# Kernel optimization log

Hardware: AMD Instinct MI355X
Metric: run time of the kernel (lower is better)

The kernel has to match this reference:

```python
import jax, jax.numpy as jnp
import numpy as np

B, S, D = 4, 2048, 1024
NEG_BIG = -1.0e9


def setup_inputs() -> dict:
    key = jax.random.key(0)
    ks = jax.random.split(key, 9)
    scale = 1.0 / np.sqrt(D)
    inp = {
        "v": jax.random.normal(ks[0], (B, S, D), dtype=jnp.float32),
        "k": jax.random.normal(ks[1], (B, S, D), dtype=jnp.float32),
        "q": jax.random.normal(ks[2], (B, S, D), dtype=jnp.float32),
        # causal mask: 1 where attention is disallowed (j > i), broadcast over batch
        "mask": jnp.triu(jnp.ones((1, S, S), dtype=jnp.float32), k=1),
        "Wq": jax.random.normal(ks[3], (D, D), dtype=jnp.float32) * scale,
        "bq": jnp.zeros((D,), dtype=jnp.float32),
        "Wk": jax.random.normal(ks[4], (D, D), dtype=jnp.float32) * scale,
        "bk": jnp.zeros((D,), dtype=jnp.float32),
        "Wv": jax.random.normal(ks[5], (D, D), dtype=jnp.float32) * scale,
        "bv": jnp.zeros((D,), dtype=jnp.float32),
    }
    return inp


def reference(v, k, q, mask, Wq, bq, Wk, bk, Wv, bv):
    # Dense projections (Keras Dense: x @ W + b)
    qp = q @ Wq + bq  # [B, S, D]
    kp = k @ Wk + bk  # [B, S, D]
    vp = v @ Wv + bv  # [B, S, D]

    dk = jnp.asarray(D, dtype=qp.dtype)
    logits = jnp.einsum("bqd,bkd->bqk", qp, kp) / jnp.sqrt(dk)  # [B, S, S]
    logits = logits + mask * NEG_BIG
    attn = jax.nn.softmax(logits, axis=-1)  # [B, S, S]
    out = jnp.einsum("bqk,bkd->bqd", attn, vp)  # [B, S, D]
    return out, attn
```

## Files before the change

### kernel.cpp

```cpp
#include <hip/hip_runtime.h>
#include <hip/hip_bf16.h>
#include <cstdint>

#define BATCH 4
#define S_LEN 2048
#define D_DIM 1024

typedef __attribute__((ext_vector_type(4))) float f32x4_t;
typedef __attribute__((ext_vector_type(8))) __bf16 bf16x8_t;

__device__ __forceinline__ ushort f32_to_bf16(float f) {
    uint32_t u = __float_as_uint(f);
    uint32_t r = (u + 0x7FFFu + ((u >> 16) & 1u)) >> 16;
    return (ushort)r;
}

__global__ __launch_bounds__(256)
void cvt3_kernel(const float* __restrict__ a, const float* __restrict__ b,
                 const float* __restrict__ c, ushort* __restrict__ out, int n4) {
    int z = blockIdx.y;
    const float* src = (z == 0) ? a : ((z == 1) ? b : c);
    ushort* dst = out + (size_t)z * n4 * 4;
    int idx = blockIdx.x * blockDim.x + threadIdx.x;
    int stride = gridDim.x * blockDim.x;
    const float4* in4 = (const float4*)src;
    ushort4* out4 = (ushort4*)dst;
    for (int i = idx; i < n4; i += stride) {
        float4 v = in4[i];
        ushort4 o;
        o.x = f32_to_bf16(v.x);
        o.y = f32_to_bf16(v.y);
        o.z = f32_to_bf16(v.z);
        o.w = f32_to_bf16(v.w);
        out4[i] = o;
    }
}

__global__ __launch_bounds__(256)
void transpose_cvt_kernel(const float* __restrict__ in, ushort* __restrict__ out,
                          int rows, int cols) {
    __shared__ ushort tile[64][66];
    int r0 = blockIdx.y * 64, c0 = blockIdx.x * 64;
    int t = threadIdx.x;
    int cr = t & 63;
    int cc = t >> 6;
    #pragma unroll
    for (int i = 0; i < 16; ++i) {
        int r = cc * 16 + i;
        tile[r][cr] = f32_to_bf16(in[(size_t)(r0 + r) * cols + (c0 + cr)]);
    }
    __syncthreads();
    #pragma unroll
    for (int i = 0; i < 16; ++i) {
        int c = cc * 16 + i;
        out[(size_t)(c0 + c) * rows + (r0 + cr)] = tile[cr][c];
    }
}

__global__ __launch_bounds__(256)
void transpose_bf16_kernel(const ushort* __restrict__ in, ushort* __restrict__ out,
                           int rows, int cols, int lda, long strideA, long strideB) {
    __shared__ ushort tile[64][66];
    const ushort* src = in + (size_t)blockIdx.z * strideA;
    ushort* dst = out + (size_t)blockIdx.z * strideB;
    int r0 = blockIdx.y * 64, c0 = blockIdx.x * 64;
    int t = threadIdx.x;
    int cr = t & 63;
    int cc = t >> 6;
    #pragma unroll
    for (int i = 0; i < 16; ++i) {
        int r = cc * 16 + i;
        tile[r][cr] = src[(size_t)(r0 + r) * lda + (c0 + cr)];
    }
    __syncthreads();
    #pragma unroll
    for (int i = 0; i < 16; ++i) {
        int c = cc * 16 + i;
        dst[(size_t)(c0 + c) * rows + (r0 + cr)] = tile[cr][c];
    }
}

enum { MODE_PROJ = 0, MODE_LOGITS = 1, MODE_OUT = 2 };

#define GBM 128
#define GBN 128
#define GBK 32

template<int MODE>
__global__ __launch_bounds__(256)
void gemm_bt_kernel(const ushort* __restrict__ A, const ushort* __restrict__ Bt,
                    const float* __restrict__ bias, void* __restrict__ Cout,
                    int K, int lda, int ldb, int ldc,
                    long strideA, long strideB, long strideC, float scale) {
    int bc = blockIdx.x, br = blockIdx.y, bz = blockIdx.z;
    if (MODE == MODE_LOGITS && bc > br) return;

    __shared__ ushort As[2][GBM * GBK];
    __shared__ ushort Bs[2][GBN * GBK];

    const ushort* Ab = (MODE == MODE_PROJ) ? A + (size_t)(bc >> 3) * strideA
                                           : A + (size_t)bz * strideA;
    const ushort* Bb = Bt + (size_t)bz * strideB;

    int brow = br * GBM, bcol = bc * GBN;
    int t = threadIdx.x;
    int lane = t & 63;
    int wave = t >> 6;
    int wr = wave >> 1, wc = wave & 1;

    int ksteps = K / GBK;
    if (MODE == MODE_OUT) ksteps = min(ksteps, (brow + GBM) / GBK);

    f32x4_t acc[4][4];
    #pragma unroll
    for (int m = 0; m < 4; ++m)
        #pragma unroll
        for (int n = 0; n < 4; ++n)
            acc[m][n] = (f32x4_t){0.f, 0.f, 0.f, 0.f};

    int row0 = t >> 2;
    int col0 = (t & 3) * 8;

    auto stage = [&](int kt, int buf) {
        int k0 = kt * GBK;
        #pragma unroll
        for (int i = 0; i < 2; ++i) {
            int row = i * 64 + row0;
            const ushort* srcA = Ab + (size_t)(brow + row) * lda + (k0 + col0);
            __builtin_amdgcn_global_load_lds(
                (const __attribute__((address_space(1))) uint32_t*)srcA,
                (__attribute__((address_space(3))) uint32_t*)&As[buf][(i * 256 + t) * 8],
                16, 0, 0);
            const ushort* srcB = Bb + (size_t)(bcol + row) * ldb + (k0 + col0);
            __builtin_amdgcn_global_load_lds(
                (const __attribute__((address_space(1))) uint32_t*)srcB,
                (__attribute__((address_space(3))) uint32_t*)&Bs[buf][(i * 256 + t) * 8],
                16, 0, 0);
        }
    };

    stage(0, 0);
    __syncthreads();

    for (int kt = 0; kt < ksteps; ++kt) {
        int cur = kt & 1;
        if (kt + 1 < ksteps) stage(kt + 1, cur ^ 1);

        bf16x8_t a_frag[4], b_frag[4];
        int arow = wr * 64 + (lane & 15);
        int kcol = (lane >> 4) * 8;
        #pragma unroll
        for (int m = 0; m < 4; ++m)
            a_frag[m] = *(const bf16x8_t*)&As[cur][(arow + m * 16) * GBK + kcol];
        int brl = wc * 64 + (lane & 15);
        #pragma unroll
        for (int n = 0; n < 4; ++n)
            b_frag[n] = *(const bf16x8_t*)&Bs[cur][(brl + n * 16) * GBK + kcol];

        __builtin_amdgcn_s_setprio(1);
        #pragma unroll
        for (int m = 0; m < 4; ++m)
            #pragma unroll
            for (int n = 0; n < 4; ++n)
                acc[m][n] = __builtin_amdgcn_mfma_f32_16x16x32_bf16(
                    a_frag[m], b_frag[n], acc[m][n], 0, 0, 0);
        __builtin_amdgcn_s_setprio(0);

        __syncthreads();
    }

    int crow0 = brow + wr * 64 + ((lane >> 4) * 4);
    int ccol0 = bcol + wc * 64 + (lane & 15);
    if (MODE == MODE_PROJ) {
        ushort* C = (ushort*)Cout;
        #pragma unroll
        for (int m = 0; m < 4; ++m) {
            #pragma unroll
            for (int n = 0; n < 4; ++n) {
                int col = ccol0 + n * 16;
                float bv = bias[col];
                #pragma unroll
                for (int j = 0; j < 4; ++j) {
                    int rowg = crow0 + m * 16 + j;
                    C[(size_t)rowg * ldc + col] = f32_to_bf16(acc[m][n][j] + bv);
                }
            }
        }
    } else {
        float* C = (float*)Cout + (size_t)bz * strideC;
        #pragma unroll
        for (int m = 0; m < 4; ++m)
            #pragma unroll
            for (int n = 0; n < 4; ++n) {
                int col = ccol0 + n * 16;
                #pragma unroll
                for (int j = 0; j < 4; ++j) {
                    int rowg = crow0 + m * 16 + j;
                    C[(size_t)rowg * ldc + col] = acc[m][n][j] * scale;
                }
            }
    }
}

__global__ __launch_bounds__(256)
void bias_concat_kernel(const float* __restrict__ bq, const float* __restrict__ bk,
                        const float* __restrict__ bv, float* __restrict__ out) {
    int i = blockIdx.x * blockDim.x + threadIdx.x;
    if (i < D_DIM) out[i] = bq[i];
    else if (i < 2 * D_DIM) out[i] = bk[i - D_DIM];
    else if (i < 3 * D_DIM) out[i] = bv[i - 2 * D_DIM];
}

__global__ __launch_bounds__(256)
void softmax_causal_kernel(float* __restrict__ attn, ushort* __restrict__ attn_bf) {
    int rowid = blockIdx.x;
    int i = rowid & (S_LEN - 1);
    float* lrow = attn + (size_t)rowid * S_LEN;
    ushort* brw = attn_bf + (size_t)rowid * S_LEN;
    int t = threadIdx.x;
    int nvalid = i + 1;

    float vals[8];
    float lmax = -1e30f;
    #pragma unroll
    for (int it = 0; it < 8; ++it) {
        int j = it * 256 + t;
        float v = (j < nvalid) ? lrow[j] : -1e30f;
        vals[it] = v;
        lmax = fmaxf(lmax, v);
    }
    #pragma unroll
    for (int off = 32; off > 0; off >>= 1)
        lmax = fmaxf(lmax, __shfl_xor(lmax, off));

    __shared__ float redm[4];
    __shared__ float reds[4];
    int wave = t >> 6, lane = t & 63;
    if (lane == 0) redm[wave] = lmax;
    __syncthreads();
    float m = fmaxf(fmaxf(redm[0], redm[1]), fmaxf(redm[2], redm[3]));

    float lsum = 0.f;
    #pragma unroll
    for (int it = 0; it < 8; ++it) {
        int j = it * 256 + t;
        float e = (j < nvalid) ? __expf(vals[it] - m) : 0.f;
        vals[it] = e;
        lsum += e;
    }
    #pragma unroll
    for (int off = 32; off > 0; off >>= 1)
        lsum += __shfl_xor(lsum, off);
    if (lane == 0) reds[wave] = lsum;
    __syncthreads();
    float denom = reds[0] + reds[1] + reds[2] + reds[3];
    float inv = 1.f / denom;

    #pragma unroll
    for (int it = 0; it < 8; ++it) {
        int j = it * 256 + t;
        float p = vals[it] * inv;
        lrow[j] = p;
        brw[j] = f32_to_bf16(p);
    }
}

extern "C" void kernel_launch(void* const* d_in, const int* in_sizes, int n_in,
                              void* d_out, int out_size, void* d_ws, size_t ws_size,
                              hipStream_t stream) {
    const float* v  = (const float*)d_in[0];
    const float* k  = (const float*)d_in[1];
    const float* q  = (const float*)d_in[2];
    const float* Wq = (const float*)d_in[4];
    const float* bq = (const float*)d_in[5];
    const float* Wk = (const float*)d_in[6];
    const float* bk = (const float*)d_in[7];
    const float* Wv = (const float*)d_in[8];
    const float* bv = (const float*)d_in[9];

    float* out  = (float*)d_out;
    float* attn = (float*)d_out + (size_t)BATCH * S_LEN * D_DIM;

    char* ws = (char*)d_ws;
    const size_t NTOK = (size_t)BATCH * S_LEN;
    const size_t XSZ  = NTOK * D_DIM * sizeof(ushort);
    ushort* xqkv  = (ushort*)(ws);
    ushort* qkvp  = (ushort*)(ws + 3 * XSZ);
    ushort* WT    = (ushort*)(ws + 6 * XSZ);
    float*  bias3 = (float*)(ws + 6 * XSZ + 3 * (size_t)D_DIM * D_DIM * sizeof(ushort));
    ushort* vpT     = (ushort*)(ws);
    ushort* attn_bf = (ushort*)(ws + XSZ);

    const int n4 = (int)(NTOK * D_DIM / 4);
    cvt3_kernel<<<dim3(1024, 3), dim3(256), 0, stream>>>(q, k, v, xqkv, n4);

    transpose_cvt_kernel<<<dim3(16, 16), dim3(256), 0, stream>>>(Wq, WT, D_DIM, D_DIM);
    transpose_cvt_kernel<<<dim3(16, 16), dim3(256), 0, stream>>>(Wk, WT + (size_t)D_DIM * D_DIM, D_DIM, D_DIM);
    transpose_cvt_kernel<<<dim3(16, 16), dim3(256), 0, stream>>>(Wv, WT + 2 * (size_t)D_DIM * D_DIM, D_DIM, D_DIM);
    bias_concat_kernel<<<dim3(12), dim3(256), 0, stream>>>(bq, bk, bv, bias3);

    dim3 pgrid(3 * D_DIM / GBN, (int)(NTOK / GBM), 1);
    gemm_bt_kernel<MODE_PROJ><<<pgrid, dim3(256), 0, stream>>>(
        xqkv, WT, bias3, qkvp, D_DIM, D_DIM, D_DIM, 3 * D_DIM,
        (long)NTOK * D_DIM, 0, 0, 1.f);

    transpose_bf16_kernel<<<dim3(D_DIM / 64, S_LEN / 64, BATCH), dim3(256), 0, stream>>>(
        qkvp + 2 * D_DIM, vpT, S_LEN, D_DIM, 3 * D_DIM,
        (long)S_LEN * 3 * D_DIM, (long)D_DIM * S_LEN);

    dim3 lgrid(S_LEN / GBN, S_LEN / GBM, BATCH);
    gemm_bt_kernel<MODE_LOGITS><<<lgrid, dim3(256), 0, stream>>>(
        qkvp, qkvp + D_DIM, nullptr, attn, D_DIM, 3 * D_DIM, 3 * D_DIM, S_LEN,
        (long)S_LEN * 3 * D_DIM, (long)S_LEN * 3 * D_DIM, (long)S_LEN * S_LEN, 0.03125f);

    softmax_causal_kernel<<<dim3((int)NTOK), dim3(256), 0, stream>>>(attn, attn_bf);

    dim3 ogrid(D_DIM / GBN, S_LEN / GBM, BATCH);
    gemm_bt_kernel<MODE_OUT><<<ogrid, dim3(256), 0, stream>>>(
        attn_bf, vpT, nullptr, out, S_LEN, S_LEN, S_LEN, D_DIM,
        (long)S_LEN * S_LEN, (long)D_DIM * S_LEN, (long)S_LEN * D_DIM, 1.f);
}
```

Baseline: 243.1 us.

## Rewrite GEMM with 256x128x64 tiles, 3-stage LDS pipeline and XOR swizzle

Replaces the 128x128x32 double-buffered GEMM with a 512-thread 256x128x64 tile kernel. It uses a triple-buffered LDS ring filled by async global_load_lds, XOR-swizzled LDS addressing to avoid bank conflicts, and split stage/compute phases with explicit waitcnt and barriers. The aim is more reuse per tile, better hiding of load latency, and less LDS bank-conflict stall. In exchange it uses much more LDS (occupancy 1), produces fewer blocks for the smaller GEMMs, and adds coarser causal skipping that wastes more work on the triangular logits.

```diff
diff --git a/kernel.cpp b/kernel.cpp
--- a/kernel.cpp
+++ b/kernel.cpp
@@ -80,103 +80,164 @@
     }
 }
 
+__global__ __launch_bounds__(256)
+void bias_concat_kernel(const float* __restrict__ bq, const float* __restrict__ bk,
+                        const float* __restrict__ bv, float* __restrict__ out) {
+    int i = blockIdx.x * blockDim.x + threadIdx.x;
+    if (i < D_DIM) out[i] = bq[i];
+    else if (i < 2 * D_DIM) out[i] = bk[i - D_DIM];
+    else if (i < 3 * D_DIM) out[i] = bv[i - 2 * D_DIM];
+}
+
 enum { MODE_PROJ = 0, MODE_LOGITS = 1, MODE_OUT = 2 };
 
-#define GBM 128
-#define GBN 128
-#define GBK 32
+#define BM 256
+#define BN 128
+#define BK 64
+#define NSLOT 3
 
 template<int MODE>
-__global__ __launch_bounds__(256)
-void gemm_bt_kernel(const ushort* __restrict__ A, const ushort* __restrict__ Bt,
-                    const float* __restrict__ bias, void* __restrict__ Cout,
-                    int K, int lda, int ldb, int ldc,
-                    long strideA, long strideB, long strideC, float scale) {
+__global__ __launch_bounds__(512, 1)
+void gemm3_kernel(const ushort* __restrict__ A, const ushort* __restrict__ Bt,
+                  const float* __restrict__ bias, void* __restrict__ Cout,
+                  int K, int lda, int ldb, int ldc,
+                  long strideA, long strideB, long strideC, float scale) {
     int bc = blockIdx.x, br = blockIdx.y, bz = blockIdx.z;
-    if (MODE == MODE_LOGITS && bc > br) return;
-
-    __shared__ ushort As[2][GBM * GBK];
-    __shared__ ushort Bs[2][GBN * GBK];
+    if (MODE == MODE_LOGITS && bc >= 2 * (br + 1)) return;
+
+    __shared__ ushort As[NSLOT][BM * BK];
+    __shared__ ushort Bs[NSLOT][BN * BK];
 
     const ushort* Ab = (MODE == MODE_PROJ) ? A + (size_t)(bc >> 3) * strideA
                                            : A + (size_t)bz * strideA;
     const ushort* Bb = Bt + (size_t)bz * strideB;
 
-    int brow = br * GBM, bcol = bc * GBN;
+    int brow = br * BM, bcol = bc * BN;
     int t = threadIdx.x;
     int lane = t & 63;
-    int wave = t >> 6;
-    int wr = wave >> 1, wc = wave & 1;
-
-    int ksteps = K / GBK;
-    if (MODE == MODE_OUT) ksteps = min(ksteps, (brow + GBM) / GBK);
-
-    f32x4_t acc[4][4];
-    #pragma unroll
-    for (int m = 0; m < 4; ++m)
-        #pragma unroll
-        for (int n = 0; n < 4; ++n)
+    int wid = t >> 6;
+    int wr = wid >> 2, wc = wid & 3;
+
+    int nkt = K / BK;
+    if (MODE == MODE_OUT) nkt = min(nkt, (brow + BM) / BK);
+
+    auto stageA = [&](int kt, int slot, int j) {
+        int o = (j * 512 + t) * 16;
+        int row = o >> 7;
+        int col = (o & 127) ^ ((row & 7) << 4);
+        const ushort* src = Ab + (size_t)(brow + row) * lda + kt * BK + (col >> 1);
+        __builtin_amdgcn_global_load_lds(
+            (const __attribute__((address_space(1))) uint32_t*)src,
+            (__attribute__((address_space(3))) uint32_t*)&As[slot][o >> 1],
+            16, 0, 0);
+    };
+    auto stageB = [&](int kt, int slot, int j) {
+        int o = (j * 512 + t) * 16;
+        int row = o >> 7;
+        int col = (o & 127) ^ ((row & 7) << 4);
+        const ushort* src = Bb + (size_t)(bcol + row) * ldb + kt * BK + (col >> 1);
+        __builtin_amdgcn_global_load_lds(
+            (const __attribute__((address_space(1))) uint32_t*)src,
+            (__attribute__((address_space(3))) uint32_t*)&Bs[slot][o >> 1],
+            16, 0, 0);
+    };
+
+    f32x4_t acc[8][2];
+    #pragma unroll
+    for (int m = 0; m < 8; ++m)
+        #pragma unroll
+        for (int n = 0; n < 2; ++n)
             acc[m][n] = (f32x4_t){0.f, 0.f, 0.f, 0.f};
 
-    int row0 = t >> 2;
-    int col0 = (t & 3) * 8;
-
-    auto stage = [&](int kt, int buf) {
-        int k0 = kt * GBK;
-        #pragma unroll
-        for (int i = 0; i < 2; ++i) {
-            int row = i * 64 + row0;
-            const ushort* srcA = Ab + (size_t)(brow + row) * lda + (k0 + col0);
-            __builtin_amdgcn_global_load_lds(
-                (const __attribute__((address_space(1))) uint32_t*)srcA,
-                (__attribute__((address_space(3))) uint32_t*)&As[buf][(i * 256 + t) * 8],
-                16, 0, 0);
-            const ushort* srcB = Bb + (size_t)(bcol + row) * ldb + (k0 + col0);
-            __builtin_amdgcn_global_load_lds(
-                (const __attribute__((address_space(1))) uint32_t*)srcB,
-                (__attribute__((address_space(3))) uint32_t*)&Bs[buf][(i * 256 + t) * 8],
-                16, 0, 0);
+    bf16x8_t af[4][2], bf[2][2];
+
+    auto readA = [&](int slot, int mh) {
+        #pragma unroll
+        for (int m = 0; m < 4; ++m) {
+            int ra = wr * 128 + mh * 64 + m * 16 + (lane & 15);
+            int sw = (ra & 7) << 4;
+            #pragma unroll
+            for (int ks = 0; ks < 2; ++ks) {
+                int cb = ks * 64 + ((lane >> 4) * 16);
+                af[m][ks] = *(const bf16x8_t*)((const char*)&As[slot][0] + ra * 128 + (cb ^ sw));
+            }
         }
     };
-
-    stage(0, 0);
-    __syncthreads();
-
-    for (int kt = 0; kt < ksteps; ++kt) {
-        int cur = kt & 1;
-        if (kt + 1 < ksteps) stage(kt + 1, cur ^ 1);
-
-        bf16x8_t a_frag[4], b_frag[4];
-        int arow = wr * 64 + (lane & 15);
-        int kcol = (lane >> 4) * 8;
+    auto readB = [&](int slot) {
+        #pragma unroll
+        for (int n = 0; n < 2; ++n) {
+            int rb = wc * 32 + n * 16 + (lane & 15);
+            int sw = (rb & 7) << 4;
+            #pragma unroll
+            for (int ks = 0; ks < 2; ++ks) {
+                int cb = ks * 64 + ((lane >> 4) * 16);
+                bf[n][ks] = *(const bf16x8_t*)((const char*)&Bs[slot][0] + rb * 128 + (cb ^ sw));
+            }
+        }
+    };
+
+    #pragma unroll
+    for (int j = 0; j < 4; ++j) stageA(0, 0, j);
+    stageB(0, 0, 0); stageB(0, 0, 1);
+    #pragma unroll
+    for (int j = 0; j < 4; ++j) stageA(1, 1, j);
+    stageB(1, 1, 0); stageB(1, 1, 1);
+    asm volatile("s_waitcnt vmcnt(6)" ::: "memory");
+    __builtin_amdgcn_sched_barrier(0);
+    __builtin_amdgcn_s_barrier();
+
+    int slot = 0;
+    for (int kt = 0; kt < nkt; ++kt) {
+        int sslot = slot + 2; if (sslot >= NSLOT) sslot -= NSLOT;
+        bool dostage = (kt + 2 < nkt);
+
+        if (dostage) { stageA(kt + 2, sslot, 0); stageA(kt + 2, sslot, 1); stageB(kt + 2, sslot, 0); }
+        readB(slot);
+        readA(slot, 0);
+        asm volatile("s_waitcnt lgkmcnt(0)" ::: "memory");
+        __builtin_amdgcn_sched_barrier(0);
+        __builtin_amdgcn_s_setprio(1);
         #pragma unroll
         for (int m = 0; m < 4; ++m)
-            a_frag[m] = *(const bf16x8_t*)&As[cur][(arow + m * 16) * GBK + kcol];
-        int brl = wc * 64 + (lane & 15);
-        #pragma unroll
-        for (int n = 0; n < 4; ++n)
-            b_frag[n] = *(const bf16x8_t*)&Bs[cur][(brl + n * 16) * GBK + kcol];
-
+            #pragma unroll
+            for (int n = 0; n < 2; ++n)
+                #pragma unroll
+                for (int ks = 0; ks < 2; ++ks)
+                    acc[m][n] = __builtin_amdgcn_mfma_f32_16x16x32_bf16(
+                        af[m][ks], bf[n][ks], acc[m][n], 0, 0, 0);
+        __builtin_amdgcn_s_setprio(0);
+        __builtin_amdgcn_s_barrier();
+
+        if (dostage) { stageA(kt + 2, sslot, 2); stageA(kt + 2, sslot, 3); stageB(kt + 2, sslot, 1); }
+        readA(slot, 1);
+        asm volatile("s_waitcnt lgkmcnt(0)" ::: "memory");
+        __builtin_amdgcn_sched_barrier(0);
         __builtin_amdgcn_s_setprio(1);
         #pragma unroll
         for (int m = 0; m < 4; ++m)
             #pragma unroll
-            for (int n = 0; n < 4; ++n)
-                acc[m][n] = __builtin_amdgcn_mfma_f32_16x16x32_bf16(
-                    a_frag[m], b_frag[n], acc[m][n], 0, 0, 0);
+            for (int n = 0; n < 2; ++n)
+                #pragma unroll
+                for (int ks = 0; ks < 2; ++ks)
+                    acc[4 + m][n] = __builtin_amdgcn_mfma_f32_16x16x32_bf16(
+                        af[m][ks], bf[n][ks], acc[4 + m][n], 0, 0, 0);
         __builtin_amdgcn_s_setprio(0);
-
-        __syncthreads();
-    }
-
-    int crow0 = brow + wr * 64 + ((lane >> 4) * 4);
-    int ccol0 = bcol + wc * 64 + (lane & 15);
+        if (dostage) { asm volatile("s_waitcnt vmcnt(6)" ::: "memory"); }
+        else         { asm volatile("s_waitcnt vmcnt(0)" ::: "memory"); }
+        __builtin_amdgcn_sched_barrier(0);
+        __builtin_amdgcn_s_barrier();
+
+        slot += 1; if (slot >= NSLOT) slot -= NSLOT;
+    }
+
+    int crow0 = brow + wr * 128 + ((lane >> 4) * 4);
+    int ccol0 = bcol + wc * 32 + (lane & 15);
     if (MODE == MODE_PROJ) {
         ushort* C = (ushort*)Cout;
         #pragma unroll
-        for (int m = 0; m < 4; ++m) {
-            #pragma unroll
-            for (int n = 0; n < 4; ++n) {
+        for (int m = 0; m < 8; ++m) {
+            #pragma unroll
+            for (int n = 0; n < 2; ++n) {
                 int col = ccol0 + n * 16;
                 float bv = bias[col];
                 #pragma unroll
@@ -189,9 +250,9 @@
     } else {
         float* C = (float*)Cout + (size_t)bz * strideC;
         #pragma unroll
-        for (int m = 0; m < 4; ++m)
-            #pragma unroll
-            for (int n = 0; n < 4; ++n) {
+        for (int m = 0; m < 8; ++m)
+            #pragma unroll
+            for (int n = 0; n < 2; ++n) {
                 int col = ccol0 + n * 16;
                 #pragma unroll
                 for (int j = 0; j < 4; ++j) {
@@ -200,15 +261,6 @@
                 }
             }
     }
-}
-
-__global__ __launch_bounds__(256)
-void bias_concat_kernel(const float* __restrict__ bq, const float* __restrict__ bk,
-                        const float* __restrict__ bv, float* __restrict__ out) {
-    int i = blockIdx.x * blockDim.x + threadIdx.x;
-    if (i < D_DIM) out[i] = bq[i];
-    else if (i < 2 * D_DIM) out[i] = bk[i - D_DIM];
-    else if (i < 3 * D_DIM) out[i] = bv[i - 2 * D_DIM];
 }
 
 __global__ __launch_bounds__(256)
@@ -299,8 +351,8 @@
     transpose_cvt_kernel<<<dim3(16, 16), dim3(256), 0, stream>>>(Wv, WT + 2 * (size_t)D_DIM * D_DIM, D_DIM, D_DIM);
     bias_concat_kernel<<<dim3(12), dim3(256), 0, stream>>>(bq, bk, bv, bias3);
 
-    dim3 pgrid(3 * D_DIM / GBN, (int)(NTOK / GBM), 1);
-    gemm_bt_kernel<MODE_PROJ><<<pgrid, dim3(256), 0, stream>>>(
+    dim3 pgrid(3 * D_DIM / BN, (int)(NTOK / BM), 1);
+    gemm3_kernel<MODE_PROJ><<<pgrid, dim3(512), 0, stream>>>(
         xqkv, WT, bias3, qkvp, D_DIM, D_DIM, D_DIM, 3 * D_DIM,
         (long)NTOK * D_DIM, 0, 0, 1.f);
 
@@ -308,15 +360,15 @@
         qkvp + 2 * D_DIM, vpT, S_LEN, D_DIM, 3 * D_DIM,
         (long)S_LEN * 3 * D_DIM, (long)D_DIM * S_LEN);
 
-    dim3 lgrid(S_LEN / GBN, S_LEN / GBM, BATCH);
-    gemm_bt_kernel<MODE_LOGITS><<<lgrid, dim3(256), 0, stream>>>(
+    dim3 lgrid(S_LEN / BN, S_LEN / BM, BATCH);
+    gemm3_kernel<MODE_LOGITS><<<lgrid, dim3(512), 0, stream>>>(
         qkvp, qkvp + D_DIM, nullptr, attn, D_DIM, 3 * D_DIM, 3 * D_DIM, S_LEN,
         (long)S_LEN * 3 * D_DIM, (long)S_LEN * 3 * D_DIM, (long)S_LEN * S_LEN, 0.03125f);
 
     softmax_causal_kernel<<<dim3((int)NTOK), dim3(256), 0, stream>>>(attn, attn_bf);
 
-    dim3 ogrid(D_DIM / GBN, S_LEN / GBM, BATCH);
-    gemm_bt_kernel<MODE_OUT><<<ogrid, dim3(256), 0, stream>>>(
+    dim3 ogrid(D_DIM / BN, S_LEN / BM, BATCH);
+    gemm3_kernel<MODE_OUT><<<ogrid, dim3(512), 0, stream>>>(
         attn_bf, vpT, nullptr, out, S_LEN, S_LEN, S_LEN, D_DIM,
         (long)S_LEN * S_LEN, (long)D_DIM * S_LEN, (long)S_LEN * D_DIM, 1.f);
 }
```

Result: slower. 282.2 us (+16.1%).

## Replace generic GEMM with larger-tile swizzled, interleaved-pipeline MFMA kernels

Applied to the files above, without the earlier changes.

Replaces the 128x128x32 GEMM with two kernels using 256x256 or 256x128 tiles, BK=64, 512 threads, XOR-swizzled LDS layout, and an XCD-aware block remap. The main loop interleaves global->LDS staging with MFMA quadrants using explicit barriers and vmcnt gates. This aims for more data reuse per tile, fewer LDS bank conflicts, better L2 locality and better overlap of loads with compute. It raises register and LDS use per block and depends on hand-tuned waitcnt ordering being correct.

```diff
diff --git a/kernel.cpp b/kernel.cpp
--- a/kernel.cpp
+++ b/kernel.cpp
@@ -80,128 +80,6 @@
     }
 }
 
-enum { MODE_PROJ = 0, MODE_LOGITS = 1, MODE_OUT = 2 };
-
-#define GBM 128
-#define GBN 128
-#define GBK 32
-
-template<int MODE>
-__global__ __launch_bounds__(256)
-void gemm_bt_kernel(const ushort* __restrict__ A, const ushort* __restrict__ Bt,
-                    const float* __restrict__ bias, void* __restrict__ Cout,
-                    int K, int lda, int ldb, int ldc,
-                    long strideA, long strideB, long strideC, float scale) {
-    int bc = blockIdx.x, br = blockIdx.y, bz = blockIdx.z;
-    if (MODE == MODE_LOGITS && bc > br) return;
-
-    __shared__ ushort As[2][GBM * GBK];
-    __shared__ ushort Bs[2][GBN * GBK];
-
-    const ushort* Ab = (MODE == MODE_PROJ) ? A + (size_t)(bc >> 3) * strideA
-                                           : A + (size_t)bz * strideA;
-    const ushort* Bb = Bt + (size_t)bz * strideB;
-
-    int brow = br * GBM, bcol = bc * GBN;
-    int t = threadIdx.x;
-    int lane = t & 63;
-    int wave = t >> 6;
-    int wr = wave >> 1, wc = wave & 1;
-
-    int ksteps = K / GBK;
-    if (MODE == MODE_OUT) ksteps = min(ksteps, (brow + GBM) / GBK);
-
-    f32x4_t acc[4][4];
-    #pragma unroll
-    for (int m = 0; m < 4; ++m)
-        #pragma unroll
-        for (int n = 0; n < 4; ++n)
-            acc[m][n] = (f32x4_t){0.f, 0.f, 0.f, 0.f};
-
-    int row0 = t >> 2;
-    int col0 = (t & 3) * 8;
-
-    auto stage = [&](int kt, int buf) {
-        int k0 = kt * GBK;
-        #pragma unroll
-        for (int i = 0; i < 2; ++i) {
-            int row = i * 64 + row0;
-            const ushort* srcA = Ab + (size_t)(brow + row) * lda + (k0 + col0);
-            __builtin_amdgcn_global_load_lds(
-                (const __attribute__((address_space(1))) uint32_t*)srcA,
-                (__attribute__((address_space(3))) uint32_t*)&As[buf][(i * 256 + t) * 8],
-                16, 0, 0);
-            const ushort* srcB = Bb + (size_t)(bcol + row) * ldb + (k0 + col0);
-            __builtin_amdgcn_global_load_lds(
-                (const __attribute__((address_space(1))) uint32_t*)srcB,
-                (__attribute__((address_space(3))) uint32_t*)&Bs[buf][(i * 256 + t) * 8],
-                16, 0, 0);
-        }
-    };
-
-    stage(0, 0);
-    __syncthreads();
-
-    for (int kt = 0; kt < ksteps; ++kt) {
-        int cur = kt & 1;
-        if (kt + 1 < ksteps) stage(kt + 1, cur ^ 1);
-
-        bf16x8_t a_frag[4], b_frag[4];
-        int arow = wr * 64 + (lane & 15);
-        int kcol = (lane >> 4) * 8;
-        #pragma unroll
-        for (int m = 0; m < 4; ++m)
-            a_frag[m] = *(const bf16x8_t*)&As[cur][(arow + m * 16) * GBK + kcol];
-        int brl = wc * 64 + (lane & 15);
-        #pragma unroll
-        for (int n = 0; n < 4; ++n)
-            b_frag[n] = *(const bf16x8_t*)&Bs[cur][(brl + n * 16) * GBK + kcol];
-
-        __builtin_amdgcn_s_setprio(1);
-        #pragma unroll
-        for (int m = 0; m < 4; ++m)
-            #pragma unroll
-            for (int n = 0; n < 4; ++n)
-                acc[m][n] = __builtin_amdgcn_mfma_f32_16x16x32_bf16(
-                    a_frag[m], b_frag[n], acc[m][n], 0, 0, 0);
-        __builtin_amdgcn_s_setprio(0);
-
-        __syncthreads();
-    }
-
-    int crow0 = brow + wr * 64 + ((lane >> 4) * 4);
-    int ccol0 = bcol + wc * 64 + (lane & 15);
-    if (MODE == MODE_PROJ) {
-        ushort* C = (ushort*)Cout;
-        #pragma unroll
-        for (int m = 0; m < 4; ++m) {
-            #pragma unroll
-            for (int n = 0; n < 4; ++n) {
-                int col = ccol0 + n * 16;
-                float bv = bias[col];
-                #pragma unroll
-                for (int j = 0; j < 4; ++j) {
-                    int rowg = crow0 + m * 16 + j;
-                    C[(size_t)rowg * ldc + col] = f32_to_bf16(acc[m][n][j] + bv);
-                }
-            }
-        }
-    } else {
-        float* C = (float*)Cout + (size_t)bz * strideC;
-        #pragma unroll
-        for (int m = 0; m < 4; ++m)
-            #pragma unroll
-            for (int n = 0; n < 4; ++n) {
-                int col = ccol0 + n * 16;
-                #pragma unroll
-                for (int j = 0; j < 4; ++j) {
-                    int rowg = crow0 + m * 16 + j;
-                    C[(size_t)rowg * ldc + col] = acc[m][n][j] * scale;
-                }
-            }
-    }
-}
-
 __global__ __launch_bounds__(256)
 void bias_concat_kernel(const float* __restrict__ bq, const float* __restrict__ bk,
                         const float* __restrict__ bv, float* __restrict__ out) {
@@ -209,6 +87,302 @@
     if (i < D_DIM) out[i] = bq[i];
     else if (i < 2 * D_DIM) out[i] = bk[i - D_DIM];
     else if (i < 3 * D_DIM) out[i] = bv[i - 2 * D_DIM];
+}
+
+enum { MODE_PROJ = 0, MODE_LOGITS = 1, MODE_OUT = 2 };
+
+#define PRE_BAR() do { __builtin_amdgcn_sched_barrier(0); __builtin_amdgcn_s_barrier(); \
+    asm volatile("s_waitcnt lgkmcnt(0)" ::: "memory"); __builtin_amdgcn_sched_barrier(0); } while (0)
+#define POST_BAR() do { __builtin_amdgcn_sched_barrier(0); __builtin_amdgcn_s_barrier(); } while (0)
+#define GATE(N) do { asm volatile("s_waitcnt vmcnt(" #N ")" ::: "memory"); \
+    __builtin_amdgcn_sched_barrier(0); } while (0)
+
+__device__ __forceinline__ void xcd_swizzle(int& bc, int& br) {
+    int gx = gridDim.x;
+    int nwg = gx * gridDim.y;
+    int orig = blockIdx.y * gx + blockIdx.x;
+    int xcd = orig & 7, idx = orig >> 3;
+    int q8 = nwg >> 3, r8 = nwg & 7;
+    int wgid = (xcd < r8 ? xcd * (q8 + 1) : r8 * (q8 + 1) + (xcd - r8) * q8) + idx;
+    bc = wgid % gx;
+    br = wgid / gx;
+}
+
+__global__ __launch_bounds__(512, 2)
+void gemm_proj_kernel(const ushort* __restrict__ A, const ushort* __restrict__ Bt,
+                      const float* __restrict__ bias, ushort* __restrict__ Cout,
+                      int K, int lda, int ldb, int ldc, long strideA) {
+    __shared__ ushort As[2][256 * 64];
+    __shared__ ushort Bs[2][256 * 64];
+    int bc, br;
+    xcd_swizzle(bc, br);
+    const ushort* Ab = A + (size_t)(bc >> 2) * strideA;
+    const ushort* Bb = Bt;
+    int brow = br * 256, bcol = bc * 256;
+    int t = threadIdx.x, lane = t & 63, wid = t >> 6;
+    int wr = wid >> 2, wc = wid & 3;
+    int nkt = K / 64, niter = nkt >> 1;
+
+    auto stageA = [&](int tk, int half) {
+        ushort* dst = &As[tk & 1][0];
+        #pragma unroll
+        for (int j = 0; j < 2; ++j) {
+            int o = half * 16384 + (j * 512 + t) * 16;
+            int row = o >> 7;
+            int col = (o & 127) ^ ((row & 7) << 4);
+            const ushort* src = Ab + (size_t)(brow + row) * lda + tk * 64 + (col >> 1);
+            __builtin_amdgcn_global_load_lds(
+                (const __attribute__((address_space(1))) uint32_t*)src,
+                (__attribute__((address_space(3))) uint32_t*)(dst + (o >> 1)), 16, 0, 0);
+        }
+    };
+    auto stageB = [&](int tk, int half) {
+        ushort* dst = &Bs[tk & 1][0];
+        #pragma unroll
+        for (int j = 0; j < 2; ++j) {
+            int o = half * 16384 + (j * 512 + t) * 16;
+            int row = o >> 7;
+            int col = (o & 127) ^ ((row & 7) << 4);
+            const ushort* src = Bb + (size_t)(bcol + row) * ldb + tk * 64 + (col >> 1);
+            __builtin_amdgcn_global_load_lds(
+                (const __attribute__((address_space(1))) uint32_t*)src,
+                (__attribute__((address_space(3))) uint32_t*)(dst + (o >> 1)), 16, 0, 0);
+        }
+    };
+
+    f32x4_t acc[8][4];
+    #pragma unroll
+    for (int m = 0; m < 8; ++m)
+        #pragma unroll
+        for (int n = 0; n < 4; ++n)
+            acc[m][n] = (f32x4_t){0.f, 0.f, 0.f, 0.f};
+
+    bf16x8_t afl[4][2], afh[4][2], bfr[4][2];
+
+    auto readAhalf = [&](int tk, int mh, bf16x8_t (&dst)[4][2]) {
+        const char* base = (const char*)&As[tk & 1][0];
+        #pragma unroll
+        for (int m = 0; m < 4; ++m) {
+            int ra = wr * 128 + mh * 64 + m * 16 + (lane & 15);
+            int sw = (ra & 7) << 4;
+            #pragma unroll
+            for (int ks = 0; ks < 2; ++ks) {
+                int cb = ks * 64 + ((lane >> 4) * 16);
+                dst[m][ks] = *(const bf16x8_t*)(base + ra * 128 + (cb ^ sw));
+            }
+        }
+    };
+    auto readB = [&](int tk) {
+        const char* base = (const char*)&Bs[tk & 1][0];
+        #pragma unroll
+        for (int n = 0; n < 4; ++n) {
+            int rb = wc * 64 + n * 16 + (lane & 15);
+            int sw = (rb & 7) << 4;
+            #pragma unroll
+            for (int ks = 0; ks < 2; ++ks) {
+                int cb = ks * 64 + ((lane >> 4) * 16);
+                bfr[n][ks] = *(const bf16x8_t*)(base + rb * 128 + (cb ^ sw));
+            }
+        }
+    };
+
+#define QUAD66(AF, MH, NH)                                                          \
+    do { __builtin_amdgcn_s_setprio(1);                                             \
+        _Pragma("unroll") for (int m = 0; m < 4; ++m)                               \
+        _Pragma("unroll") for (int n = 0; n < 2; ++n)                               \
+        _Pragma("unroll") for (int ks = 0; ks < 2; ++ks)                            \
+            acc[(MH) * 4 + m][(NH) * 2 + n] = __builtin_amdgcn_mfma_f32_16x16x32_bf16( \
+                AF[m][ks], bfr[(NH) * 2 + n][ks], acc[(MH) * 4 + m][(NH) * 2 + n], 0, 0, 0); \
+        __builtin_amdgcn_s_setprio(0); } while (0)
+
+    stageA(0, 0); stageA(0, 1); stageB(0, 0); stageB(0, 1);
+    stageA(1, 0); stageA(1, 1);
+    GATE(4);
+    __builtin_amdgcn_s_barrier();
+
+    for (int i = 0; i < niter; ++i) {
+        int t2 = 2 * i, u = 2 * i + 1;
+        bool smid = (t2 + 2 < nkt);
+        readAhalf(t2, 0, afl); readB(t2);
+        stageB(u, 0);
+        PRE_BAR(); QUAD66(afl, 0, 0); POST_BAR();
+        readAhalf(t2, 1, afh);
+        stageB(u, 1);
+        PRE_BAR(); QUAD66(afl, 0, 1); POST_BAR();
+        if (smid) stageA(t2 + 2, 0);
+        PRE_BAR(); QUAD66(afh, 1, 0); POST_BAR();
+        if (smid) stageA(t2 + 2, 1);
+        PRE_BAR(); QUAD66(afh, 1, 1);
+        if (smid) { GATE(4); } else { GATE(0); }
+        POST_BAR();
+        readAhalf(u, 0, afl); readB(u);
+        if (smid) stageB(t2 + 2, 0);
+        PRE_BAR(); QUAD66(afl, 0, 0); POST_BAR();
+        readAhalf(u, 1, afh);
+        if (smid) stageB(t2 + 2, 1);
+        PRE_BAR(); QUAD66(afl, 0, 1); POST_BAR();
+        if (smid) stageA(u + 2, 0);
+        PRE_BAR(); QUAD66(afh, 1, 0); POST_BAR();
+        if (smid) stageA(u + 2, 1);
+        PRE_BAR(); QUAD66(afh, 1, 1);
+        if (smid) { GATE(4); } else { GATE(0); }
+        POST_BAR();
+    }
+#undef QUAD66
+
+    int crow0 = brow + wr * 128 + ((lane >> 4) * 4);
+    int ccol0 = bcol + wc * 64 + (lane & 15);
+    #pragma unroll
+    for (int mf = 0; mf < 8; ++mf) {
+        #pragma unroll
+        for (int nf = 0; nf < 4; ++nf) {
+            int col = ccol0 + nf * 16;
+            float bv = bias[col];
+            #pragma unroll
+            for (int j = 0; j < 4; ++j) {
+                int rowg = crow0 + mf * 16 + j;
+                Cout[(size_t)rowg * ldc + col] = f32_to_bf16(acc[mf][nf][j] + bv);
+            }
+        }
+    }
+}
+
+template<int MODE>
+__global__ __launch_bounds__(512, 2)
+void gemm_128_kernel(const ushort* __restrict__ A, const ushort* __restrict__ Bt,
+                     float* __restrict__ Cout,
+                     int K, int lda, int ldb, int ldc,
+                     long strideA, long strideB, long strideC, float scale) {
+    __shared__ ushort As[2][256 * 64];
+    __shared__ ushort Bs[2][128 * 64];
+    int bc, br;
+    xcd_swizzle(bc, br);
+    int bz = blockIdx.z;
+    if (MODE == MODE_LOGITS && bc > 2 * br + 1) return;
+    const ushort* Ab = A + (size_t)bz * strideA;
+    const ushort* Bb = Bt + (size_t)bz * strideB;
+    int brow = br * 256, bcol = bc * 128;
+    int t = threadIdx.x, lane = t & 63, wid = t >> 6;
+    int wr = wid >> 1, wc = wid & 1;
+    int nkt = K / 64;
+    if (MODE == MODE_OUT) nkt = min(nkt, (brow + 256) / 64);
+    int niter = nkt >> 1;
+
+    auto stageA = [&](int tk, int half) {
+        ushort* dst = &As[tk & 1][0];
+        #pragma unroll
+        for (int j = 0; j < 2; ++j) {
+            int o = half * 16384 + (j * 512 + t) * 16;
+            int row = o >> 7;
+            int col = (o & 127) ^ ((row & 7) << 4);
+            const ushort* src = Ab + (size_t)(brow + row) * lda + tk * 64 + (col >> 1);
+            __builtin_amdgcn_global_load_lds(
+                (const __attribute__((address_space(1))) uint32_t*)src,
+                (__attribute__((address_space(3))) uint32_t*)(dst + (o >> 1)), 16, 0, 0);
+        }
+    };
+    auto stageB = [&](int tk) {
+        ushort* dst = &Bs[tk & 1][0];
+        #pragma unroll
+        for (int j = 0; j < 2; ++j) {
+            int o = (j * 512 + t) * 16;
+            int row = o >> 7;
+            int col = (o & 127) ^ ((row & 7) << 4);
+            const ushort* src = Bb + (size_t)(bcol + row) * ldb + tk * 64 + (col >> 1);
+            __builtin_amdgcn_global_load_lds(
+                (const __attribute__((address_space(1))) uint32_t*)src,
+                (__attribute__((address_space(3))) uint32_t*)(dst + (o >> 1)), 16, 0, 0);
+        }
+    };
+
+    f32x4_t acc[4][4];
+    #pragma unroll
+    for (int m = 0; m < 4; ++m)
+        #pragma unroll
+        for (int n = 0; n < 4; ++n)
+            acc[m][n] = (f32x4_t){0.f, 0.f, 0.f, 0.f};
+
+    bf16x8_t af[4][2], bfr[4][2];
+
+    auto readAll = [&](int tk) {
+        const char* baseA = (const char*)&As[tk & 1][0];
+        #pragma unroll
+        for (int m = 0; m < 4; ++m) {
+            int ra = wr * 64 + m * 16 + (lane & 15);
+            int sw = (ra & 7) << 4;
+            #pragma unroll
+            for (int ks = 0; ks < 2; ++ks) {
+                int cb = ks * 64 + ((lane >> 4) * 16);
+                af[m][ks] = *(const bf16x8_t*)(baseA + ra * 128 + (cb ^ sw));
+            }
+        }
+        const char* baseB = (const char*)&Bs[tk & 1][0];
+        #pragma unroll
+        for (int n = 0; n < 4; ++n) {
+            int rb = wc * 64 + n * 16 + (lane & 15);
+            int sw = (rb & 7) << 4;
+            #pragma unroll
+            for (int ks = 0; ks < 2; ++ks) {
+                int cb = ks * 64 + ((lane >> 4) * 16);
+                bfr[n][ks] = *(const bf16x8_t*)(baseB + rb * 128 + (cb ^ sw));
+            }
+        }
+    };
+
+#define QUAD28(MH, NH)                                                              \
+    do { __builtin_amdgcn_s_setprio(1);                                             \
+        _Pragma("unroll") for (int m = 0; m < 2; ++m)                               \
+        _Pragma("unroll") for (int n = 0; n < 2; ++n)                               \
+        _Pragma("unroll") for (int ks = 0; ks < 2; ++ks)                            \
+            acc[(MH) * 2 + m][(NH) * 2 + n] = __builtin_amdgcn_mfma_f32_16x16x32_bf16( \
+                af[(MH) * 2 + m][ks], bfr[(NH) * 2 + n][ks], acc[(MH) * 2 + m][(NH) * 2 + n], 0, 0, 0); \
+        __builtin_amdgcn_s_setprio(0); } while (0)
+
+    stageA(0, 0); stageA(0, 1); stageB(0);
+    stageA(1, 0); stageA(1, 1); stageB(1);
+    GATE(6);
+    __builtin_amdgcn_s_barrier();
+
+    for (int i = 0; i < niter; ++i) {
+        int t2 = 2 * i, u = 2 * i + 1;
+        bool smid = (t2 + 2 < nkt);
+        readAll(t2);
+        PRE_BAR(); QUAD28(0, 0); POST_BAR();
+        PRE_BAR(); QUAD28(0, 1); POST_BAR();
+        if (smid) stageA(t2 + 2, 0);
+        PRE_BAR(); QUAD28(1, 0); POST_BAR();
+        if (smid) stageA(t2 + 2, 1);
+        PRE_BAR(); QUAD28(1, 1);
+        if (smid) { GATE(4); } else { GATE(0); }
+        POST_BAR();
+        readAll(u);
+        if (smid) stageB(t2 + 2);
+        PRE_BAR(); QUAD28(0, 0); POST_BAR();
+        if (smid) stageA(u + 2, 0);
+        PRE_BAR(); QUAD28(0, 1); POST_BAR();
+        if (smid) stageA(u + 2, 1);
+        PRE_BAR(); QUAD28(1, 0); POST_BAR();
+        if (smid) stageB(u + 2);
+        PRE_BAR(); QUAD28(1, 1);
+        if (smid) { GATE(6); } else { GATE(0); }
+        POST_BAR();
+    }
+#undef QUAD28
+
+    float* C = Cout + (size_t)bz * strideC;
+    int crow0 = brow + wr * 64 + ((lane >> 4) * 4);
+    int ccol0 = bcol + wc * 64 + (lane & 15);
+    #pragma unroll
+    for (int mf = 0; mf < 4; ++mf)
+        #pragma unroll
+        for (int nf = 0; nf < 4; ++nf) {
+            int col = ccol0 + nf * 16;
+            #pragma unroll
+            for (int j = 0; j < 4; ++j) {
+                int rowg = crow0 + mf * 16 + j;
+                C[(size_t)rowg * ldc + col] = acc[mf][nf][j] * scale;
+            }
+        }
 }
 
 __global__ __launch_bounds__(256)
@@ -299,24 +473,20 @@
     transpose_cvt_kernel<<<dim3(16, 16), dim3(256), 0, stream>>>(Wv, WT + 2 * (size_t)D_DIM * D_DIM, D_DIM, D_DIM);
     bias_concat_kernel<<<dim3(12), dim3(256), 0, stream>>>(bq, bk, bv, bias3);
 
-    dim3 pgrid(3 * D_DIM / GBN, (int)(NTOK / GBM), 1);
-    gemm_bt_kernel<MODE_PROJ><<<pgrid, dim3(256), 0, stream>>>(
-        xqkv, WT, bias3, qkvp, D_DIM, D_DIM, D_DIM, 3 * D_DIM,
-        (long)NTOK * D_DIM, 0, 0, 1.f);
+    gemm_proj_kernel<<<dim3(12, 32, 1), dim3(512), 0, stream>>>(
+        xqkv, WT, bias3, qkvp, D_DIM, D_DIM, D_DIM, 3 * D_DIM, (long)NTOK * D_DIM);
 
     transpose_bf16_kernel<<<dim3(D_DIM / 64, S_LEN / 64, BATCH), dim3(256), 0, stream>>>(
         qkvp + 2 * D_DIM, vpT, S_LEN, D_DIM, 3 * D_DIM,
         (long)S_LEN * 3 * D_DIM, (long)D_DIM * S_LEN);
 
-    dim3 lgrid(S_LEN / GBN, S_LEN / GBM, BATCH);
-    gemm_bt_kernel<MODE_LOGITS><<<lgrid, dim3(256), 0, stream>>>(
-        qkvp, qkvp + D_DIM, nullptr, attn, D_DIM, 3 * D_DIM, 3 * D_DIM, S_LEN,
+    gemm_128_kernel<MODE_LOGITS><<<dim3(16, 8, BATCH), dim3(512), 0, stream>>>(
+        qkvp, qkvp + D_DIM, attn, D_DIM, 3 * D_DIM, 3 * D_DIM, S_LEN,
         (long)S_LEN * 3 * D_DIM, (long)S_LEN * 3 * D_DIM, (long)S_LEN * S_LEN, 0.03125f);
 
     softmax_causal_kernel<<<dim3((int)NTOK), dim3(256), 0, stream>>>(attn, attn_bf);
 
-    dim3 ogrid(D_DIM / GBN, S_LEN / GBM, BATCH);
-    gemm_bt_kernel<MODE_OUT><<<ogrid, dim3(256), 0, stream>>>(
-        attn_bf, vpT, nullptr, out, S_LEN, S_LEN, S_LEN, D_DIM,
+    gemm_128_kernel<MODE_OUT><<<dim3(8, 8, BATCH), dim3(512), 0, stream>>>(
+        attn_bf, vpT, out, S_LEN, S_LEN, S_LEN, D_DIM,
         (long)S_LEN * S_LEN, (long)D_DIM * S_LEN, (long)S_LEN * D_DIM, 1.f);
 }
```

Result: no change. 242.6 us (-0.2%).

## Replace GEMM with triple-buffered 256x128 tile kernel using swizzled LDS and XCD remap

Applied to the files above, without the earlier changes.

Replaces the double-buffered 128x128x32 GEMM with a 512-thread kernel that computes 256x128 tiles at K-step 64. It triple-buffers LDS loads with explicit vmcnt/lgkmcnt gating, and XOR-swizzles the LDS layout to avoid bank conflicts. Register fragments are double-buffered so ds_reads for the next tile overlap the MFMAs, and workgroup IDs are remapped so neighbouring tiles share an XCD's L2. The intent is to raise MFMA utilization and cut LDS and global-load stalls for all three GEMMs. The trade-offs are much more LDS and register pressure and coarser causal tile skipping.

```diff
diff --git a/kernel.cpp b/kernel.cpp
--- a/kernel.cpp
+++ b/kernel.cpp
@@ -80,128 +80,6 @@
     }
 }
 
-enum { MODE_PROJ = 0, MODE_LOGITS = 1, MODE_OUT = 2 };
-
-#define GBM 128
-#define GBN 128
-#define GBK 32
-
-template<int MODE>
-__global__ __launch_bounds__(256)
-void gemm_bt_kernel(const ushort* __restrict__ A, const ushort* __restrict__ Bt,
-                    const float* __restrict__ bias, void* __restrict__ Cout,
-                    int K, int lda, int ldb, int ldc,
-                    long strideA, long strideB, long strideC, float scale) {
-    int bc = blockIdx.x, br = blockIdx.y, bz = blockIdx.z;
-    if (MODE == MODE_LOGITS && bc > br) return;
-
-    __shared__ ushort As[2][GBM * GBK];
-    __shared__ ushort Bs[2][GBN * GBK];
-
-    const ushort* Ab = (MODE == MODE_PROJ) ? A + (size_t)(bc >> 3) * strideA
-                                           : A + (size_t)bz * strideA;
-    const ushort* Bb = Bt + (size_t)bz * strideB;
-
-    int brow = br * GBM, bcol = bc * GBN;
-    int t = threadIdx.x;
-    int lane = t & 63;
-    int wave = t >> 6;
-    int wr = wave >> 1, wc = wave & 1;
-
-    int ksteps = K / GBK;
-    if (MODE == MODE_OUT) ksteps = min(ksteps, (brow + GBM) / GBK);
-
-    f32x4_t acc[4][4];
-    #pragma unroll
-    for (int m = 0; m < 4; ++m)
-        #pragma unroll
-        for (int n = 0; n < 4; ++n)
-            acc[m][n] = (f32x4_t){0.f, 0.f, 0.f, 0.f};
-
-    int row0 = t >> 2;
-    int col0 = (t & 3) * 8;
-
-    auto stage = [&](int kt, int buf) {
-        int k0 = kt * GBK;
-        #pragma unroll
-        for (int i = 0; i < 2; ++i) {
-            int row = i * 64 + row0;
-            const ushort* srcA = Ab + (size_t)(brow + row) * lda + (k0 + col0);
-            __builtin_amdgcn_global_load_lds(
-                (const __attribute__((address_space(1))) uint32_t*)srcA,
-                (__attribute__((address_space(3))) uint32_t*)&As[buf][(i * 256 + t) * 8],
-                16, 0, 0);
-            const ushort* srcB = Bb + (size_t)(bcol + row) * ldb + (k0 + col0);
-            __builtin_amdgcn_global_load_lds(
-                (const __attribute__((address_space(1))) uint32_t*)srcB,
-                (__attribute__((address_space(3))) uint32_t*)&Bs[buf][(i * 256 + t) * 8],
-                16, 0, 0);
-        }
-    };
-
-    stage(0, 0);
-    __syncthreads();
-
-    for (int kt = 0; kt < ksteps; ++kt) {
-        int cur = kt & 1;
-        if (kt + 1 < ksteps) stage(kt + 1, cur ^ 1);
-
-        bf16x8_t a_frag[4], b_frag[4];
-        int arow = wr * 64 + (lane & 15);
-        int kcol = (lane >> 4) * 8;
-        #pragma unroll
-        for (int m = 0; m < 4; ++m)
-            a_frag[m] = *(const bf16x8_t*)&As[cur][(arow + m * 16) * GBK + kcol];
-        int brl = wc * 64 + (lane & 15);
-        #pragma unroll
-        for (int n = 0; n < 4; ++n)
-            b_frag[n] = *(const bf16x8_t*)&Bs[cur][(brl + n * 16) * GBK + kcol];
-
-        __builtin_amdgcn_s_setprio(1);
-        #pragma unroll
-        for (int m = 0; m < 4; ++m)
-            #pragma unroll
-            for (int n = 0; n < 4; ++n)
-                acc[m][n] = __builtin_amdgcn_mfma_f32_16x16x32_bf16(
-                    a_frag[m], b_frag[n], acc[m][n], 0, 0, 0);
-        __builtin_amdgcn_s_setprio(0);
-
-        __syncthreads();
-    }
-
-    int crow0 = brow + wr * 64 + ((lane >> 4) * 4);
-    int ccol0 = bcol + wc * 64 + (lane & 15);
-    if (MODE == MODE_PROJ) {
-        ushort* C = (ushort*)Cout;
-        #pragma unroll
-        for (int m = 0; m < 4; ++m) {
-            #pragma unroll
-            for (int n = 0; n < 4; ++n) {
-                int col = ccol0 + n * 16;
-                float bv = bias[col];
-                #pragma unroll
-                for (int j = 0; j < 4; ++j) {
-                    int rowg = crow0 + m * 16 + j;
-                    C[(size_t)rowg * ldc + col] = f32_to_bf16(acc[m][n][j] + bv);
-                }
-            }
-        }
-    } else {
-        float* C = (float*)Cout + (size_t)bz * strideC;
-        #pragma unroll
-        for (int m = 0; m < 4; ++m)
-            #pragma unroll
-            for (int n = 0; n < 4; ++n) {
-                int col = ccol0 + n * 16;
-                #pragma unroll
-                for (int j = 0; j < 4; ++j) {
-                    int rowg = crow0 + m * 16 + j;
-                    C[(size_t)rowg * ldc + col] = acc[m][n][j] * scale;
-                }
-            }
-    }
-}
-
 __global__ __launch_bounds__(256)
 void bias_concat_kernel(const float* __restrict__ bq, const float* __restrict__ bk,
                         const float* __restrict__ bv, float* __restrict__ out) {
@@ -209,6 +87,201 @@
     if (i < D_DIM) out[i] = bq[i];
     else if (i < 2 * D_DIM) out[i] = bk[i - D_DIM];
     else if (i < 3 * D_DIM) out[i] = bv[i - 2 * D_DIM];
+}
+
+enum { MODE_PROJ = 0, MODE_LOGITS = 1, MODE_OUT = 2 };
+
+#define LGKM(N) do { asm volatile("s_waitcnt lgkmcnt(" #N ")" ::: "memory"); \
+    __builtin_amdgcn_sched_barrier(0); } while (0)
+#define GATE(N) do { asm volatile("s_waitcnt vmcnt(" #N ")" ::: "memory"); \
+    __builtin_amdgcn_sched_barrier(0); } while (0)
+
+#define GLOAD(dst, src) __builtin_amdgcn_global_load_lds( \
+    (const __attribute__((address_space(1))) uint32_t*)(src), \
+    (__attribute__((address_space(3))) uint32_t*)(dst), 16, 0, 0)
+
+__device__ __forceinline__ void xcd_swizzle(int& bc, int& br) {
+    int gx = gridDim.x;
+    int nwg = gx * gridDim.y;
+    int orig = blockIdx.y * gx + blockIdx.x;
+    int xcd = orig & 7, idx = orig >> 3;
+    int wgid = xcd * (nwg >> 3) + idx;
+    bc = wgid % gx;
+    br = wgid / gx;
+}
+
+template<int MODE>
+__global__ __launch_bounds__(512, 2)
+void gemm_pipe_kernel(const ushort* __restrict__ A, const ushort* __restrict__ Bt,
+                      const float* __restrict__ bias, void* __restrict__ Cout,
+                      int K, int lda, int ldb, int ldc,
+                      long strideA, long strideB, long strideC, float scale) {
+    __shared__ ushort As[3][256 * 64];
+    __shared__ ushort Bs[3][128 * 64];
+    int bc, br;
+    xcd_swizzle(bc, br);
+    int bz = blockIdx.z;
+    if (MODE == MODE_LOGITS && bc > 2 * br + 1) return;
+    const ushort* Ab = (MODE == MODE_PROJ) ? A + (size_t)(bc >> 3) * strideA
+                                           : A + (size_t)bz * strideA;
+    const ushort* Bb = Bt + (size_t)bz * strideB;
+    int brow = br * 256, bcol = bc * 128;
+    int t = threadIdx.x, lane = t & 63, wid = t >> 6;
+    int wr = wid >> 1, wc = wid & 1;
+    int nkt = K / 64;
+    if (MODE == MODE_OUT) nkt = min(nkt, (brow + 256) / 64);
+
+    const ushort* aSrc[4];
+    const ushort* bSrc[2];
+    int oA[4], oB[2];
+    #pragma unroll
+    for (int j = 0; j < 4; ++j) {
+        int o = (j * 512 + t) * 16;
+        int row = o >> 7;
+        int col = (o & 127) ^ ((row & 7) << 4);
+        oA[j] = o >> 1;
+        aSrc[j] = Ab + (size_t)(brow + row) * lda + (col >> 1);
+    }
+    #pragma unroll
+    for (int j = 0; j < 2; ++j) {
+        int o = (j * 512 + t) * 16;
+        int row = o >> 7;
+        int col = (o & 127) ^ ((row & 7) << 4);
+        oB[j] = o >> 1;
+        bSrc[j] = Bb + (size_t)(bcol + row) * ldb + (col >> 1);
+    }
+    auto stage = [&](int tk, int slot) {
+        ushort* dA = &As[slot][0];
+        ushort* dB = &Bs[slot][0];
+        #pragma unroll
+        for (int j = 0; j < 4; ++j) GLOAD(dA + oA[j], aSrc[j] + tk * 64);
+        #pragma unroll
+        for (int j = 0; j < 2; ++j) GLOAD(dB + oB[j], bSrc[j] + tk * 64);
+    };
+
+    int rdA[4][2], rdB[4][2];
+    #pragma unroll
+    for (int m = 0; m < 4; ++m) {
+        int ra = wr * 64 + m * 16 + (lane & 15);
+        #pragma unroll
+        for (int ks = 0; ks < 2; ++ks) {
+            int cb = ks * 64 + ((lane >> 4) * 16);
+            rdA[m][ks] = ra * 128 + (cb ^ ((ra & 7) << 4));
+        }
+    }
+    #pragma unroll
+    for (int n = 0; n < 4; ++n) {
+        int rb = wc * 64 + n * 16 + (lane & 15);
+        #pragma unroll
+        for (int ks = 0; ks < 2; ++ks) {
+            int cb = ks * 64 + ((lane >> 4) * 16);
+            rdB[n][ks] = rb * 128 + (cb ^ ((rb & 7) << 4));
+        }
+    }
+
+    f32x4_t acc[4][4];
+    #pragma unroll
+    for (int m = 0; m < 4; ++m)
+        #pragma unroll
+        for (int n = 0; n < 4; ++n)
+            acc[m][n] = (f32x4_t){0.f, 0.f, 0.f, 0.f};
+
+    bf16x8_t aE0[4], aE1[4], bE0[4], bE1[4];
+    bf16x8_t aO0[4], aO1[4], bO0[4], bO1[4];
+
+#define MF16(AV, BV)                                                           \
+    do { __builtin_amdgcn_s_setprio(1);                                        \
+        _Pragma("unroll") for (int m = 0; m < 4; ++m)                          \
+        _Pragma("unroll") for (int n = 0; n < 4; ++n)                          \
+            acc[m][n] = __builtin_amdgcn_mfma_f32_16x16x32_bf16(               \
+                AV[m], BV[n], acc[m][n], 0, 0, 0);                             \
+        __builtin_amdgcn_s_setprio(0); } while (0)
+
+#define TILE_BODY(X, CA0, CA1, CB0, CB1, NA0, NA1, NB0, NB1)                   \
+    do {                                                                       \
+        int x_ = (X);                                                          \
+        __builtin_amdgcn_s_barrier();             \
+        if (x_ + 2 < nkt) stage(x_ + 2, (x_ + 2) % 3);                         \
+        if (x_ + 1 < nkt) { if (x_ + 2 < nkt) { GATE(6); } else { GATE(0); } } \
+        __builtin_amdgcn_s_barrier();             \
+        {                                                                      \
+            const char* nA = (const char*)&As[(x_ + 1) % 3][0];                \
+            const char* nB = (const char*)&Bs[(x_ + 1) % 3][0];                \
+            if (x_ + 1 < nkt) {                                                \
+                _Pragma("unroll") for (int n = 0; n < 4; ++n)                  \
+                    NB0[n] = *(const bf16x8_t*)(nB + rdB[n][0]);               \
+                _Pragma("unroll") for (int m = 0; m < 4; ++m)                  \
+                    NA0[m] = *(const bf16x8_t*)(nA + rdA[m][0]);               \
+                LGKM(8);                  \
+            } else { LGKM(0); }                                                \
+            MF16(CA0, CB0);                                                    \
+            if (x_ + 1 < nkt) {                                                \
+                _Pragma("unroll") for (int n = 0; n < 4; ++n)                  \
+                    NB1[n] = *(const bf16x8_t*)(nB + rdB[n][1]);               \
+                _Pragma("unroll") for (int m = 0; m < 4; ++m)                  \
+                    NA1[m] = *(const bf16x8_t*)(nA + rdA[m][1]);               \
+            }                                                                  \
+            MF16(CA1, CB1);                                                    \
+        }                                                                      \
+    } while (0)
+
+    stage(0, 0);
+    stage(1, 1);
+    GATE(6);
+    __builtin_amdgcn_s_barrier();
+    {
+        const char* pA = (const char*)&As[0][0];
+        const char* pB = (const char*)&Bs[0][0];
+        #pragma unroll
+        for (int n = 0; n < 4; ++n) bE0[n] = *(const bf16x8_t*)(pB + rdB[n][0]);
+        #pragma unroll
+        for (int m = 0; m < 4; ++m) aE0[m] = *(const bf16x8_t*)(pA + rdA[m][0]);
+        #pragma unroll
+        for (int n = 0; n < 4; ++n) bE1[n] = *(const bf16x8_t*)(pB + rdB[n][1]);
+        #pragma unroll
+        for (int m = 0; m < 4; ++m) aE1[m] = *(const bf16x8_t*)(pA + rdA[m][1]);
+    }
+
+    int nhalf = nkt >> 1;
+    for (int it = 0; it < nhalf; ++it) {
+        int x = 2 * it;
+        TILE_BODY(x,     aE0, aE1, bE0, bE1, aO0, aO1, bO0, bO1);
+        TILE_BODY(x + 1, aO0, aO1, bO0, bO1, aE0, aE1, bE0, bE1);
+    }
+#undef TILE_BODY
+#undef MF16
+
+    int crow0 = brow + wr * 64 + ((lane >> 4) * 4);
+    int ccol0 = bcol + wc * 64 + (lane & 15);
+    if (MODE == MODE_PROJ) {
+        ushort* C = (ushort*)Cout;
+        #pragma unroll
+        for (int mf = 0; mf < 4; ++mf) {
+            #pragma unroll
+            for (int nf = 0; nf < 4; ++nf) {
+                int col = ccol0 + nf * 16;
+                float bv = bias[col];
+                #pragma unroll
+                for (int j = 0; j < 4; ++j) {
+                    int rowg = crow0 + mf * 16 + j;
+                    C[(size_t)rowg * ldc + col] = f32_to_bf16(acc[mf][nf][j] + bv);
+                }
+            }
+        }
+    } else {
+        float* C = (float*)Cout + (size_t)bz * strideC;
+        #pragma unroll
+        for (int mf = 0; mf < 4; ++mf)
+            #pragma unroll
+            for (int nf = 0; nf < 4; ++nf) {
+                int col = ccol0 + nf * 16;
+                #pragma unroll
+                for (int j = 0; j < 4; ++j) {
+                    int rowg = crow0 + mf * 16 + j;
+                    C[(size_t)rowg * ldc + col] = acc[mf][nf][j] * scale;
+                }
+            }
+    }
 }
 
 __global__ __launch_bounds__(256)
@@ -299,8 +372,7 @@
     transpose_cvt_kernel<<<dim3(16, 16), dim3(256), 0, stream>>>(Wv, WT + 2 * (size_t)D_DIM * D_DIM, D_DIM, D_DIM);
     bias_concat_kernel<<<dim3(12), dim3(256), 0, stream>>>(bq, bk, bv, bias3);
 
-    dim3 pgrid(3 * D_DIM / GBN, (int)(NTOK / GBM), 1);
-    gemm_bt_kernel<MODE_PROJ><<<pgrid, dim3(256), 0, stream>>>(
+    gemm_pipe_kernel<MODE_PROJ><<<dim3(24, 32, 1), dim3(512), 0, stream>>>(
         xqkv, WT, bias3, qkvp, D_DIM, D_DIM, D_DIM, 3 * D_DIM,
         (long)NTOK * D_DIM, 0, 0, 1.f);
 
@@ -308,15 +380,13 @@
         qkvp + 2 * D_DIM, vpT, S_LEN, D_DIM, 3 * D_DIM,
         (long)S_LEN * 3 * D_DIM, (long)D_DIM * S_LEN);
 
-    dim3 lgrid(S_LEN / GBN, S_LEN / GBM, BATCH);
-    gemm_bt_kernel<MODE_LOGITS><<<lgrid, dim3(256), 0, stream>>>(
+    gemm_pipe_kernel<MODE_LOGITS><<<dim3(16, 8, BATCH), dim3(512), 0, stream>>>(
         qkvp, qkvp + D_DIM, nullptr, attn, D_DIM, 3 * D_DIM, 3 * D_DIM, S_LEN,
         (long)S_LEN * 3 * D_DIM, (long)S_LEN * 3 * D_DIM, (long)S_LEN * S_LEN, 0.03125f);
 
     softmax_causal_kernel<<<dim3((int)NTOK), dim3(256), 0, stream>>>(attn, attn_bf);
 
-    dim3 ogrid(D_DIM / GBN, S_LEN / GBM, BATCH);
-    gemm_bt_kernel<MODE_OUT><<<ogrid, dim3(256), 0, stream>>>(
+    gemm_pipe_kernel<MODE_OUT><<<dim3(8, 8, BATCH), dim3(512), 0, stream>>>(
         attn_bf, vpT, nullptr, out, S_LEN, S_LEN, S_LEN, D_DIM,
         (long)S_LEN * S_LEN, (long)D_DIM * S_LEN, (long)S_LEN * D_DIM, 1.f);
 }
```

Measured after the change: 241.6 us. Within noise of the previous version (-0.6%).
